# Performance work log

Measured on AMD Instinct MI355X. Metric: run time of the kernel, lower is better.

The kernel has to match this reference:

```python
import jax, jax.numpy as jnp
import numpy as np

B, N, D = 512, 22, 3
H, TD, AD, L = 128, 32, 32, 4
SIGMA_DATA = 0.168
NORM_CONST = 1.0
E_IN = 2 * H + 1 + 2  # [h_i, h_j, radial, dist_sq, bond_mask]
NUM_ATOM_TYPES = 4
BONDS = [(0, 1), (1, 2), (1, 3), (1, 4), (4, 5), (4, 6), (6, 7), (6, 8), (8, 9), (8, 10),
         (10, 11), (10, 12), (10, 13), (8, 14), (14, 15), (14, 16), (16, 17), (16, 18),
         (18, 19), (18, 20), (18, 21)]
ATOM_TYPES = [0, 1, 0, 0, 1, 2, 3, 0, 1, 0, 1, 0, 0, 0, 1, 2, 3, 0, 1, 0, 0, 0]


def setup_inputs() -> dict:
    key = jax.random.key(0)
    ks = jax.random.split(key, 16)
    xt = jax.random.normal(ks[0], (B, N, D), jnp.float32)
    xt = xt - xt.mean(axis=1, keepdims=True)  # zero center of mass, per assert_mean_zero
    # EDM-style noise levels, strictly positive (log-normal as in compute_loss)
    t = jnp.exp(jax.random.normal(ks[1], (B,), jnp.float32) * 1.2 - 1.2)
    # fully connected edges without self-loops, batched with node offset b*N
    ii, jj = np.meshgrid(np.arange(N), np.arange(N), indexing='ij')
    msk = ii != jj
    ri, ci = ii[msk], jj[msk]  # (N*(N-1),)
    off = (np.arange(B) * N)[:, None]
    row = jnp.asarray((ri[None] + off).reshape(-1), jnp.int32)
    col = jnp.asarray((ci[None] + off).reshape(-1), jnp.int32)
    adj = np.zeros((N, N), np.float32)
    for a, b in BONDS:
        adj[a, b] = 1.0
        adj[b, a] = 1.0
    bond_mask = jnp.asarray(np.tile(adj[ri, ci], B)[:, None], jnp.float32)  # (E,1)
    atom_types = jnp.asarray(ATOM_TYPES, jnp.int32)

    def lin(k, fi, fo):
        return jax.random.normal(k, (fi, fo), jnp.float32) / np.sqrt(fi)

    def per_layer(k, fi, fo):
        return jax.random.normal(k, (L, fi, fo), jnp.float32) / np.sqrt(fi)

    z = lambda *s: jnp.zeros(s, jnp.float32)
    return dict(
        xt=xt, t=t,
        atom_table=jax.random.normal(ks[2], (NUM_ATOM_TYPES, AD), jnp.float32),
        bond_mask=bond_mask,
        W_in=lin(ks[3], TD + AD, H), b_in=z(H),
        ew1=per_layer(ks[4], E_IN, H), eb1=z(L, H),
        ew2=per_layer(ks[5], H, H), eb2=z(L, H),
        aw=per_layer(ks[6], H, 1), ab=z(L, 1),
        cw1=per_layer(ks[7], H, H), cb1=z(L, H),
        cw2=per_layer(ks[8], H, 1) * 0.1,  # coord head, no bias (xavier-small init)
        nw1=per_layer(ks[9], 2 * H, H), nb1=z(L, H),
        nw2=per_layer(ks[10], H, H), nb2=z(L, H),
        row=row, col=col, atom_types=atom_types,
    )


def _sinusoidal(u, dim):
    half = dim // 2
    freqs = jnp.exp(-jnp.log(10000.0) * jnp.arange(half, dtype=jnp.float32) / half)
    a = u[:, None] * freqs
    return jnp.concatenate([jnp.sin(a), jnp.cos(a)], axis=-1)


def reference(xt, t, atom_table, bond_mask, W_in, b_in, ew1, eb1, ew2, eb2,
              aw, ab, cw1, cb1, cw2, nw1, nb1, nw2, nb2, row, col, atom_types):
    BN = B * N
    act = jax.nn.silu
    # EDM preconditioning
    c_in = 1.0 / jnp.sqrt(t ** 2 + SIGMA_DATA ** 2)
    x = (xt * c_in[:, None, None]).reshape(BN, D)
    # node features: time embedding (broadcast per node) + atom-type embedding
    time_emb = jnp.repeat(_sinusoidal(jnp.log(t) / 4.0, TD), N, axis=0)  # (BN,TD)
    atom_emb = jnp.tile(atom_table[atom_types], (B, 1))                  # (BN,AD)
    h = jnp.concatenate([time_emb, atom_emb], axis=1) @ W_in + b_in      # (BN,H)
    # fixed edge attributes: squared distance at input scale + bond mask
    dist_sq0 = jnp.sum((x[row] - x[col]) ** 2, axis=1, keepdims=True)
    edge_attr = jnp.concatenate([dist_sq0, bond_mask], axis=1)           # (E,2)
    for l in range(L):
        diff = x[row] - x[col]                                           # (E,D)
        radial = jnp.sum(diff ** 2, axis=1, keepdims=True)               # (E,1)
        coord_diff = diff / (jnp.sqrt(radial) + NORM_CONST)
        m = jnp.concatenate([h[row], h[col], radial, edge_attr], axis=1)
        m = act(act(m @ ew1[l] + eb1[l]) @ ew2[l] + eb2[l])              # edge MLP (E,H)
        m = m * jax.nn.sigmoid(m @ aw[l] + ab[l])                        # attention gate
        trans = coord_diff * (act(m @ cw1[l] + cb1[l]) @ cw2[l])         # (E,D)
        x = x + jax.ops.segment_sum(trans, row, num_segments=BN)         # agg='sum'
        agg = jax.ops.segment_sum(m, row, num_segments=BN)               # (BN,H)
        h = h + (act(jnp.concatenate([h, agg], axis=1) @ nw1[l] + nb1[l]) @ nw2[l] + nb2[l])
    x_pred = x.reshape(B, N, D)
    x_pred = x_pred - x_pred.mean(axis=1, keepdims=True)                 # remove_mean
    c_skip = SIGMA_DATA ** 2 / (t ** 2 + SIGMA_DATA ** 2)
    c_out = t * SIGMA_DATA / jnp.sqrt(SIGMA_DATA ** 2 + t ** 2)
    return xt * c_skip[:, None, None] + x_pred * c_out[:, None, None]
```

## Files before the change

### kernel.cpp

```cpp
#include <hip/hip_runtime.h>
#include <math.h>

#define NB 512
#define NNODE 22
#define HH 128
#define NEDGE 462
#define NLAYER 4
#define CHUNK2 128
#define NSUP 4
#define SIG 0.168f

#define ASTR 136
#define NSTR 264
#define BSTR 72
#define SLW (128*72)
#define LSLICES 14
#define STAGE_BYTES 36864

typedef __attribute__((ext_vector_type(8))) short short8;
typedef __attribute__((ext_vector_type(4))) short short4v;
typedef __attribute__((ext_vector_type(4))) float f32x4;

#define MFMA_BF16 __builtin_amdgcn_mfma_f32_16x16x32_bf16

__device__ __forceinline__ float siluf(float v) { return v / (1.0f + __expf(-v)); }

__device__ __forceinline__ unsigned short f2bf(float x) {
  union { float f; unsigned u; } v; v.f = x;
  unsigned r = v.u + 0x7FFFu + ((v.u >> 16) & 1u);
  return (unsigned short)(r >> 16);
}
__device__ __forceinline__ float bf2f(unsigned short h) {
  union { unsigned u; float f; } v; v.u = ((unsigned)h) << 16; return v.f;
}
__device__ __forceinline__ void splitbf(float x, unsigned short& hi, unsigned short& lo) {
  union { float f; unsigned u; } v; v.f = x;
  hi = (unsigned short)(v.u >> 16);
  union { unsigned u; float f; } hv; hv.u = ((unsigned)hi) << 16;
  union { float f; unsigned u; } w; w.f = x - hv.f;
  lo = (unsigned short)(w.u >> 16);
}

__global__ void prep_weights(const float* __restrict__ ew1, const float* __restrict__ ew2,
                             const float* __restrict__ cw1, const float* __restrict__ nw1,
                             const float* __restrict__ nw2, unsigned short* __restrict__ ws)
{
  int idx = blockIdx.x * 256 + threadIdx.x;
  if (idx >= 4 * LSLICES * 128 * 72) return;
  int kk = idx % 72; int rest = idx / 72;
  int n = rest % 128; rest /= 128;
  int sl = rest % LSLICES; int l = rest / LSLICES;
  float val = 0.f;
  if (kk < 64) {
    if (sl < 4)       val = ew1[((size_t)l * 259 + sl * 64 + kk) * HH + n];
    else if (sl < 6)  val = ew2[((size_t)l * 128 + (sl - 4) * 64 + kk) * HH + n];
    else if (sl < 8)  val = cw1[((size_t)l * 128 + (sl - 6) * 64 + kk) * HH + n];
    else if (sl < 12) val = nw1[((size_t)l * 256 + (sl - 8) * 64 + kk) * HH + n];
    else              val = nw2[((size_t)l * 128 + (sl - 12) * 64 + kk) * HH + n];
  }
  unsigned short hi, lo;
  { union { float f; unsigned u; } v; v.f = val;
    hi = (unsigned short)(v.u >> 16);
    union { unsigned u; float f; } hv; hv.u = ((unsigned)hi) << 16;
    lo = f2bf(val - hv.f); }
  size_t base = ((size_t)(l * LSLICES + sl) * 2) * SLW + n * BSTR + kk;
  ws[base]       = hi;
  ws[base + SLW] = lo;
}

__global__ __launch_bounds__(512, 1)
void scorenet_kernel(
    const float* __restrict__ xt, const float* __restrict__ tt,
    const float* __restrict__ atom_table, const float* __restrict__ bond_mask,
    const float* __restrict__ W_in, const float* __restrict__ b_in,
    const float* __restrict__ ew1, const float* __restrict__ eb1,
    const float* __restrict__ eb2,
    const float* __restrict__ aw,  const float* __restrict__ ab,
    const float* __restrict__ cb1, const float* __restrict__ cw2,
    const float* __restrict__ nb1, const float* __restrict__ nb2,
    const int* __restrict__ atom_types,
    const unsigned short* __restrict__ ws,
    float* __restrict__ out)
{
  const int g    = blockIdx.x;
  const int tid  = threadIdx.x;
  const int lane = tid & 63;
  const int wv   = tid >> 6;
  const int ml   = lane & 15;
  const int q    = lane >> 4;
  const int mp   = wv >> 1;
  const int nh2  = wv & 1;
  const int mtn  = wv & 1;
  const int nqn  = wv >> 1;

  __shared__ __align__(16) unsigned short sh_B[2 * SLW];
  __shared__ __align__(16) unsigned short sh_Ah[CHUNK2 * ASTR];
  __shared__ __align__(16) unsigned short sh_Al[CHUNK2 * ASTR];
  __shared__ float sh_Phi[2][NNODE * HH];
  __shared__ float sh_h[NNODE * HH];
  __shared__ float sh_agg[NNODE * HH];
  __shared__ float sh_tail[8 * HH];
  __shared__ float sh_awl[HH], sh_cw2l[HH];
  __shared__ float sh_x[NNODE][3], sh_xacc[NNODE][3];
  __shared__ float sh_d0[NEDGE];
  __shared__ unsigned char sh_ei[NEDGE];
  __shared__ unsigned char sh_ej[NEDGE];
  __shared__ float sh_cd[3][CHUNK2];
  __shared__ float sh_red[CHUNK2][2];
  __shared__ float sh_gate[CHUNK2];
  __shared__ float sh_tf[32], sh_scal[2], sh_mean[3];

  auto issueB = [&](const unsigned short* src) {
    const char* s8 = (const char*)src;
    char* dbase = (char*)&sh_B[0];
    for (int base = wv * 1024; base < STAGE_BYTES; base += 8192) {
      __builtin_amdgcn_global_load_lds(
          (const __attribute__((address_space(1))) unsigned int*)(s8 + base + lane * 16),
          (__attribute__((address_space(3))) unsigned int*)(dbase + base),
          16, 0, 0);
    }
  };

  auto gemmE = [&](f32x4 (&acc)[2][4], int koff) {
    int arow0 = (mp * 32 + ml) * ASTR + koff;
    int arow1 = arow0 + 16 * ASTR;
#pragma unroll
    for (int sb = 0; sb < 2; sb++) {
      int k8 = sb * 32 + q * 8;
      short8 ah0 = *(const short8*)&sh_Ah[arow0 + k8];
      short8 al0 = *(const short8*)&sh_Al[arow0 + k8];
      short8 ah1 = *(const short8*)&sh_Ah[arow1 + k8];
      short8 al1 = *(const short8*)&sh_Al[arow1 + k8];
#pragma unroll
      for (int t = 0; t < 4; t++) {
        int bi = ((nh2 * 4 + t) * 16 + ml) * BSTR + k8;
        short8 bh = *(const short8*)&sh_B[bi];
        short8 bl = *(const short8*)&sh_B[SLW + bi];
        acc[0][t] = MFMA_BF16(ah0, bh, acc[0][t], 0, 0, 0);
        acc[0][t] = MFMA_BF16(ah0, bl, acc[0][t], 0, 0, 0);
        acc[0][t] = MFMA_BF16(al0, bh, acc[0][t], 0, 0, 0);
        acc[1][t] = MFMA_BF16(ah1, bh, acc[1][t], 0, 0, 0);
        acc[1][t] = MFMA_BF16(ah1, bl, acc[1][t], 0, 0, 0);
        acc[1][t] = MFMA_BF16(al1, bh, acc[1][t], 0, 0, 0);
      }
    }
  };

  auto gemmN = [&](f32x4 (&acc)[2], int astr, int koff) {
#pragma unroll
    for (int sb = 0; sb < 2; sb++) {
      int ak = (mtn * 16 + ml) * astr + koff + sb * 32 + q * 8;
      short8 ah = *(const short8*)&sh_Ah[ak];
      short8 al = *(const short8*)&sh_Al[ak];
#pragma unroll
      for (int tt = 0; tt < 2; tt++) {
        int bi = ((nqn * 2 + tt) * 16 + ml) * BSTR + sb * 32 + q * 8;
        short8 bh = *(const short8*)&sh_B[bi];
        short8 bl = *(const short8*)&sh_B[SLW + bi];
        acc[tt] = MFMA_BF16(ah, bh, acc[tt], 0, 0, 0);
        acc[tt] = MFMA_BF16(ah, bl, acc[tt], 0, 0, 0);
        acc[tt] = MFMA_BF16(al, bh, acc[tt], 0, 0, 0);
      }
    }
  };

  if (tid == 0) {
    float tg = tt[g];
    sh_scal[0] = rsqrtf(tg * tg + SIG * SIG);
    sh_scal[1] = tg;
  }
  __syncthreads();
  const float c_in = sh_scal[0];
  for (int idx = tid; idx < NNODE * 3; idx += 512) {
    sh_x[idx / 3][idx % 3] = xt[(size_t)g * NNODE * 3 + idx] * c_in;
    sh_xacc[idx / 3][idx % 3] = 0.f;
  }
  if (tid < 32) {
    float u = __logf(sh_scal[1]) * 0.25f;
    int   qq = tid & 15;
    float f = __expf((float)qq * -0.5756462732485115f);
    float a = u * f;
    sh_tf[tid] = (tid < 16) ? __sinf(a) : __cosf(a);
  }
  for (int idx = tid; idx < CHUNK2 * ASTR / 2; idx += 512) {
    ((unsigned*)sh_Ah)[idx] = 0u; ((unsigned*)sh_Al)[idx] = 0u;
  }
  __syncthreads();
  for (int o = tid; o < HH; o += 512) {
    float s = b_in[o];
#pragma unroll 8
    for (int k = 0; k < 32; k++) s += sh_tf[k] * W_in[k * HH + o];
    sh_agg[o] = s;
  }
  for (int idx = tid; idx < 4 * HH; idx += 512) {
    int a = idx >> 7, o = idx & 127;
    float s = 0.f;
#pragma unroll 8
    for (int k = 0; k < 32; k++) s += atom_table[a * 32 + k] * W_in[(32 + k) * HH + o];
    sh_agg[(1 + a) * HH + o] = s;
  }
  for (int e = tid; e < NEDGE; e += 512) {
    int i = e / 21; int r = e - i * 21; int jn = r + (r >= i);
    float bm = bond_mask[(size_t)g * NEDGE + e];
    sh_ei[e] = (unsigned char)(i | ((bm != 0.f) ? 0x80 : 0));
    sh_ej[e] = (unsigned char)jn;
    float dx = sh_x[i][0] - sh_x[jn][0];
    float dy = sh_x[i][1] - sh_x[jn][1];
    float dz = sh_x[i][2] - sh_x[jn][2];
    sh_d0[e] = dx * dx + dy * dy + dz * dz;
  }
  __syncthreads();
  for (int idx = tid; idx < NNODE * HH; idx += 512) {
    int n = idx >> 7, o = idx & 127;
    int at = atom_types[n];
    sh_h[idx] = sh_agg[o] + sh_agg[(1 + at) * HH + o];
  }
  issueB(ws);
  __syncthreads();
  for (int idx = tid; idx < NNODE * HH; idx += 512) sh_agg[idx] = 0.f;

  const f32x4 zf = {0.f, 0.f, 0.f, 0.f};

  for (int l = 0; l < NLAYER; l++) {
    const unsigned short* wsL = ws + (size_t)l * LSLICES * 2 * SLW;
    const float abl = ab[l];

    for (int idx = tid; idx < 8 * HH; idx += 512) {
      int rsel = idx >> 7, n = idx & 127;
      float v;
      switch (rsel) {
        case 0: v = ew1[((size_t)l * 259 + 256) * HH + n]; break;
        case 1: v = ew1[((size_t)l * 259 + 257) * HH + n]; break;
        case 2: v = ew1[((size_t)l * 259 + 258) * HH + n]; break;
        case 3: v = eb1[l * HH + n]; break;
        case 4: v = eb2[l * HH + n]; break;
        case 5: v = cb1[l * HH + n]; break;
        case 6: v = nb1[l * HH + n]; break;
        default: v = nb2[l * HH + n]; break;
      }
      sh_tail[idx] = v;
    }
    if (tid < HH) sh_awl[tid] = aw[l * HH + tid];
    else if (tid < 2 * HH) sh_cw2l[tid - HH] = cw2[l * HH + (tid - HH)];
    for (int idx = tid; idx < NNODE * 16; idx += 512) {
      int nd = idx >> 4, nb = (idx & 15) * 8;
      const float* hp = &sh_h[nd * HH + nb];
      union { short8 v; unsigned short s[8]; } oh, ol;
#pragma unroll
      for (int jj = 0; jj < 8; jj++) { unsigned short hi, lo; splitbf(hp[jj], hi, lo); oh.s[jj] = hi; ol.s[jj] = lo; }
      *(short8*)&sh_Ah[nd * ASTR + nb] = oh.v;
      *(short8*)&sh_Al[nd * ASTR + nb] = ol.v;
    }
    __syncthreads();

    for (int side = 0; side < 2; side++) {
      f32x4 accP[2] = {zf, zf};
      for (int s2 = 0; s2 < 2; s2++) {
        gemmN(accP, ASTR, s2 * 64);
        __syncthreads();
        int st = side * 2 + s2;
        issueB(wsL + (st < 3 ? (st + 1) : 4) * 2 * SLW);
        if (s2 == 0) __syncthreads();
      }
#pragma unroll
      for (int tt = 0; tt < 2; tt++) {
        int col = (nqn * 2 + tt) * 16 + ml;
#pragma unroll
        for (int r = 0; r < 4; r++) {
          int row = mtn * 16 + q * 4 + r;
          if (row < NNODE) sh_Phi[side][row * HH + col] = accP[tt][r];
        }
      }
      __syncthreads();
    }

    for (int sc = 0; sc < NSUP; sc++) {
      const int e0 = sc * CHUNK2;
      {
        int nb = (tid & 15) * 8, eb_ = tid >> 4;
        for (int j4 = 0; j4 < 4; j4++) {
          int el = eb_ + 32 * j4; int e = e0 + el;
          union { short8 v; unsigned short s[8]; } oh, ol;
          if (e < NEDGE) {
            int c = sh_ei[e]; int i = c & 31; int jn = sh_ej[e];
            float bnd = (float)(c >> 7);
            float dx = sh_x[i][0] - sh_x[jn][0];
            float dy = sh_x[i][1] - sh_x[jn][1];
            float dz = sh_x[i][2] - sh_x[jn][2];
            float rad = dx * dx + dy * dy + dz * dz;
            float d0v = sh_d0[e];
            const float* pi = &sh_Phi[0][i * HH + nb];
            const float* pj = &sh_Phi[1][jn * HH + nb];
#pragma unroll
            for (int jj = 0; jj < 8; jj++) {
              float v = pi[jj] + pj[jj] +
                        rad * sh_tail[nb + jj] + d0v * sh_tail[128 + nb + jj] +
                        bnd * sh_tail[256 + nb + jj] + sh_tail[384 + nb + jj];
              unsigned short hi, lo; splitbf(siluf(v), hi, lo);
              oh.s[jj] = hi; ol.s[jj] = lo;
            }
          } else {
#pragma unroll
            for (int jj = 0; jj < 8; jj++) { oh.s[jj] = 0; ol.s[jj] = 0; }
          }
          *(short8*)&sh_Ah[el * ASTR + nb] = oh.v;
          *(short8*)&sh_Al[el * ASTR + nb] = ol.v;
        }
      }
      __syncthreads();
      f32x4 acc2[2][4];
#pragma unroll
      for (int m2i = 0; m2i < 2; m2i++)
#pragma unroll
        for (int t = 0; t < 4; t++) acc2[m2i][t] = zf;
      gemmE(acc2, 0);
      __syncthreads();
      issueB(wsL + 5 * 2 * SLW);
      if (tid < CHUNK2) {
        int e = e0 + tid;
        if (e < NEDGE) {
          int i = sh_ei[e] & 31, jn = sh_ej[e];
          float dx = sh_x[i][0] - sh_x[jn][0];
          float dy = sh_x[i][1] - sh_x[jn][1];
          float dz = sh_x[i][2] - sh_x[jn][2];
          float inv = 1.0f / (sqrtf(dx * dx + dy * dy + dz * dz) + 1.0f);
          sh_cd[0][tid] = dx * inv; sh_cd[1][tid] = dy * inv; sh_cd[2][tid] = dz * inv;
        } else {
          sh_cd[0][tid] = 0.f; sh_cd[1][tid] = 0.f; sh_cd[2][tid] = 0.f;
        }
      }
      __syncthreads();
      gemmE(acc2, 64);
      __syncthreads();
      issueB(wsL + 6 * 2 * SLW);
      {
        float gpr[2][4];
#pragma unroll
        for (int m2i = 0; m2i < 2; m2i++)
#pragma unroll
          for (int r = 0; r < 4; r++) gpr[m2i][r] = 0.f;
#pragma unroll
        for (int m2i = 0; m2i < 2; m2i++) {
#pragma unroll
          for (int t = 0; t < 4; t++) {
            int col = nh2 * 64 + t * 16 + ml;
            float eb2c = sh_tail[512 + col], awc = sh_awl[col];
#pragma unroll
            for (int r = 0; r < 4; r++) {
              float v = siluf(acc2[m2i][t][r] + eb2c);
              gpr[m2i][r] += v * awc;
              unsigned short hi, lo; splitbf(v, hi, lo);
              int ai = (mp * 32 + m2i * 16 + q * 4 + r) * ASTR + col;
              sh_Ah[ai] = hi; sh_Al[ai] = lo;
            }
          }
        }
#pragma unroll
        for (int m = 1; m < 16; m <<= 1)
#pragma unroll
          for (int m2i = 0; m2i < 2; m2i++)
#pragma unroll
            for (int r = 0; r < 4; r++) gpr[m2i][r] += __shfl_xor(gpr[m2i][r], m, 64);
        if (ml == 0) {
#pragma unroll
          for (int m2i = 0; m2i < 2; m2i++)
#pragma unroll
            for (int r = 0; r < 4; r++)
              sh_red[mp * 32 + m2i * 16 + q * 4 + r][nh2] = gpr[m2i][r];
        }
      }
      __syncthreads();
      if (tid < CHUNK2)
        sh_gate[tid] = 1.0f / (1.0f + __expf(-(sh_red[tid][0] + sh_red[tid][1] + abl)));
      f32x4 acc3[2][4];
#pragma unroll
      for (int m2i = 0; m2i < 2; m2i++)
#pragma unroll
        for (int t = 0; t < 4; t++) acc3[m2i][t] = zf;
      gemmE(acc3, 0);
      __syncthreads();
      issueB(wsL + 7 * 2 * SLW);
      int elast = ((e0 + CHUNK2 < NEDGE) ? e0 + CHUNK2 : NEDGE) - 1;
      int i_lo = e0 / 21, i_hi = elast / 21;
      int nrows = i_hi - i_lo + 1;
      for (int idx = tid; idx < nrows * 32; idx += 512) {
        int i = i_lo + (idx >> 5), fb = (idx & 31) * 4;
        int es = i * 21; if (es < e0) es = e0;
        int ee = i * 21 + 21;
        if (ee > e0 + CHUNK2) ee = e0 + CHUNK2;
        if (ee > NEDGE) ee = NEDGE;
        float* ap = &sh_agg[i * HH + fb];
        float a4[4];
#pragma unroll
        for (int c = 0; c < 4; c++) a4[c] = ap[c];
        for (int e = es; e < ee; e++) {
          float gg = sh_gate[e - e0];
          union { short4v v; unsigned short s[4]; } uh, ul;
          uh.v = *(const short4v*)&sh_Ah[(e - e0) * ASTR + fb];
          ul.v = *(const short4v*)&sh_Al[(e - e0) * ASTR + fb];
#pragma unroll
          for (int c = 0; c < 4; c++) a4[c] += gg * (bf2f(uh.s[c]) + bf2f(ul.s[c]));
        }
#pragma unroll
        for (int c = 0; c < 4; c++) ap[c] = a4[c];
      }
      __syncthreads();
      gemmE(acc3, 64);
      __syncthreads();
      issueB(sc < 3 ? wsL + 4 * 2 * SLW : wsL + 8 * 2 * SLW);
      {
        float cs[2][4];
#pragma unroll
        for (int m2i = 0; m2i < 2; m2i++) {
          float g4[4];
#pragma unroll
          for (int r = 0; r < 4; r++) {
            g4[r] = sh_gate[mp * 32 + m2i * 16 + q * 4 + r];
            cs[m2i][r] = 0.f;
          }
#pragma unroll
          for (int t = 0; t < 4; t++) {
            int col = nh2 * 64 + t * 16 + ml;
            float cb1c = sh_tail[640 + col], cwc = sh_cw2l[col];
#pragma unroll
            for (int r = 0; r < 4; r++)
              cs[m2i][r] += siluf(g4[r] * acc3[m2i][t][r] + cb1c) * cwc;
          }
        }
#pragma unroll
        for (int m = 1; m < 16; m <<= 1)
#pragma unroll
          for (int m2i = 0; m2i < 2; m2i++)
#pragma unroll
            for (int r = 0; r < 4; r++) cs[m2i][r] += __shfl_xor(cs[m2i][r], m, 64);
        if (ml == 0) {
#pragma unroll
          for (int m2i = 0; m2i < 2; m2i++)
#pragma unroll
            for (int r = 0; r < 4; r++)
              sh_red[mp * 32 + m2i * 16 + q * 4 + r][nh2] = cs[m2i][r];
        }
      }
      __syncthreads();
      for (int idx = tid; idx < nrows * 3; idx += 512) {
        int i = i_lo + idx / 3, d = idx % 3;
        int es = i * 21; if (es < e0) es = e0;
        int ee = i * 21 + 21;
        if (ee > e0 + CHUNK2) ee = e0 + CHUNK2;
        if (ee > NEDGE) ee = NEDGE;
        float s = 0.f;
        for (int e = es; e < ee; e++)
          s += sh_cd[d][e - e0] * (sh_red[e - e0][0] + sh_red[e - e0][1]);
        sh_xacc[i][d] += s;
      }
    }

    for (int idx = tid; idx < NNODE * 32; idx += 512) {
      int nd = idx >> 5, kb = (idx & 31) * 8;
      const float* src = (kb < 128) ? &sh_h[nd * HH + kb] : &sh_agg[nd * HH + (kb - 128)];
      union { short8 v; unsigned short s[8]; } oh, ol;
#pragma unroll
      for (int jj = 0; jj < 8; jj++) { unsigned short hi, lo; splitbf(src[jj], hi, lo); oh.s[jj] = hi; ol.s[jj] = lo; }
      *(short8*)&sh_Ah[nd * NSTR + kb] = oh.v;
      *(short8*)&sh_Al[nd * NSTR + kb] = ol.v;
    }
    __syncthreads();
    {
      f32x4 n1a[2] = {zf, zf};
      for (int s = 0; s < 4; s++) {
        gemmN(n1a, NSTR, s * 64);
        __syncthreads();
        issueB(wsL + (s < 3 ? (9 + s) : 12) * 2 * SLW);
        if (s < 3) __syncthreads();
      }
#pragma unroll
      for (int tt = 0; tt < 2; tt++) {
        int col = (nqn * 2 + tt) * 16 + ml;
        float nb1c = sh_tail[768 + col];
#pragma unroll
        for (int r = 0; r < 4; r++) {
          int row = mtn * 16 + q * 4 + r;
          if (row < NNODE) {
            unsigned short hi, lo; splitbf(siluf(n1a[tt][r] + nb1c), hi, lo);
            sh_Ah[row * ASTR + col] = hi; sh_Al[row * ASTR + col] = lo;
          }
        }
      }
      __syncthreads();
      f32x4 n2a[2] = {zf, zf};
      gemmN(n2a, ASTR, 0);
      __syncthreads();
      issueB(wsL + 13 * 2 * SLW);
      for (int idx = tid; idx < NNODE * 3; idx += 512) {
        int n = idx / 3, d = idx % 3;
        sh_x[n][d] += sh_xacc[n][d];
        sh_xacc[n][d] = 0.f;
      }
      for (int idx = tid; idx < NNODE * HH; idx += 512) sh_agg[idx] = 0.f;
      __syncthreads();
      gemmN(n2a, ASTR, 64);
      __syncthreads();
      if (l < 3) issueB(ws + (size_t)(l + 1) * LSLICES * 2 * SLW);
#pragma unroll
      for (int tt = 0; tt < 2; tt++) {
        int col = (nqn * 2 + tt) * 16 + ml;
        float nb2c = sh_tail[896 + col];
#pragma unroll
        for (int r = 0; r < 4; r++) {
          int row = mtn * 16 + q * 4 + r;
          if (row < NNODE) sh_h[row * HH + col] += n2a[tt][r] + nb2c;
        }
      }
    }
    __syncthreads();
  }

  if (tid < 3) {
    float s = 0.f;
    for (int n = 0; n < NNODE; n++) s += sh_x[n][tid];
    sh_mean[tid] = s * (1.0f / NNODE);
  }
  __syncthreads();
  {
    float tg = sh_scal[1];
    float den = tg * tg + SIG * SIG;
    float c_skip = (SIG * SIG) / den;
    float c_out  = tg * SIG * rsqrtf(den);
    for (int idx = tid; idx < NNODE * 3; idx += 512) {
      int n = idx / 3, d = idx % 3;
      out[(size_t)g * NNODE * 3 + idx] =
          xt[(size_t)g * NNODE * 3 + idx] * c_skip + (sh_x[n][d] - sh_mean[d]) * c_out;
    }
  }
}

extern "C" void kernel_launch(void* const* d_in, const int* in_sizes, int n_in,
                              void* d_out, int out_size, void* d_ws, size_t ws_size,
                              hipStream_t stream) {
  const float* xt         = (const float*)d_in[0];
  const float* t          = (const float*)d_in[1];
  const float* atom_table = (const float*)d_in[2];
  const float* bond_mask  = (const float*)d_in[3];
  const float* W_in       = (const float*)d_in[4];
  const float* b_in       = (const float*)d_in[5];
  const float* ew1        = (const float*)d_in[6];
  const float* eb1        = (const float*)d_in[7];
  const float* ew2        = (const float*)d_in[8];
  const float* eb2        = (const float*)d_in[9];
  const float* aw         = (const float*)d_in[10];
  const float* ab         = (const float*)d_in[11];
  const float* cw1        = (const float*)d_in[12];
  const float* cb1        = (const float*)d_in[13];
  const float* cw2        = (const float*)d_in[14];
  const float* nw1        = (const float*)d_in[15];
  const float* nb1        = (const float*)d_in[16];
  const float* nw2        = (const float*)d_in[17];
  const float* nb2        = (const float*)d_in[18];
  const int* atom_types   = (const int*)d_in[21];

  unsigned short* ws = (unsigned short*)d_ws;

  prep_weights<<<2016, 256, 0, stream>>>(ew1, ew2, cw1, nw1, nw2, ws);

  scorenet_kernel<<<NB, 512, 0, stream>>>(
      xt, t, atom_table, bond_mask, W_in, b_in,
      ew1, eb1, eb2, aw, ab, cb1, cw2, nb1, nb2,
      atom_types, ws, (float*)d_out);
}
```

Measured before the change: 703.0 us.

## Double block size to 1024 threads and re-split MFMA tiles across 16 waves

Raises the block from 8 to 16 waves and remaps the edge and node GEMM tiles so each wave owns half as many output columns, with the gate and coordinate reductions widened to four partial sums. It also drops the precomputed initial-distance array and instead recomputes the initial squared distance per edge from a saved copy of the initial coordinates. The aim is more latency hiding and MFMA parallelism per CU for the single resident block. In exchange, the register budget per thread is tighter, barrier cost rises with more waves, and each wave now loads the A fragments for only half the MFMAs.

```diff
diff --git a/kernel.cpp b/kernel.cpp
--- a/kernel.cpp
+++ b/kernel.cpp
@@ -16,6 +16,7 @@
 #define SLW (128*72)
 #define LSLICES 14
 #define STAGE_BYTES 36864
+#define NT 1024
 
 typedef __attribute__((ext_vector_type(8))) short short8;
 typedef __attribute__((ext_vector_type(4))) short short4v;
@@ -68,7 +69,7 @@
   ws[base + SLW] = lo;
 }
 
-__global__ __launch_bounds__(512, 1)
+__global__ __launch_bounds__(NT, 1)
 void scorenet_kernel(
     const float* __restrict__ xt, const float* __restrict__ tt,
     const float* __restrict__ atom_table, const float* __restrict__ bond_mask,
@@ -88,10 +89,10 @@
   const int wv   = tid >> 6;
   const int ml   = lane & 15;
   const int q    = lane >> 4;
-  const int mp   = wv >> 1;
-  const int nh2  = wv & 1;
+  const int mp   = wv >> 2;
+  const int nq   = wv & 3;
   const int mtn  = wv & 1;
-  const int nqn  = wv >> 1;
+  const int nt8  = wv >> 1;
 
   __shared__ __align__(16) unsigned short sh_B[2 * SLW];
   __shared__ __align__(16) unsigned short sh_Ah[CHUNK2 * ASTR];
@@ -101,19 +102,18 @@
   __shared__ float sh_agg[NNODE * HH];
   __shared__ float sh_tail[8 * HH];
   __shared__ float sh_awl[HH], sh_cw2l[HH];
-  __shared__ float sh_x[NNODE][3], sh_xacc[NNODE][3];
-  __shared__ float sh_d0[NEDGE];
+  __shared__ float sh_x[NNODE][3], sh_xacc[NNODE][3], sh_x0[NNODE][3];
   __shared__ unsigned char sh_ei[NEDGE];
   __shared__ unsigned char sh_ej[NEDGE];
   __shared__ float sh_cd[3][CHUNK2];
-  __shared__ float sh_red[CHUNK2][2];
+  __shared__ float sh_red[CHUNK2][4];
   __shared__ float sh_gate[CHUNK2];
   __shared__ float sh_tf[32], sh_scal[2], sh_mean[3];
 
   auto issueB = [&](const unsigned short* src) {
     const char* s8 = (const char*)src;
     char* dbase = (char*)&sh_B[0];
-    for (int base = wv * 1024; base < STAGE_BYTES; base += 8192) {
+    for (int base = wv * 1024; base < STAGE_BYTES; base += 16384) {
       __builtin_amdgcn_global_load_lds(
           (const __attribute__((address_space(1))) unsigned int*)(s8 + base + lane * 16),
           (__attribute__((address_space(3))) unsigned int*)(dbase + base),
@@ -121,7 +121,7 @@
     }
   };
 
-  auto gemmE = [&](f32x4 (&acc)[2][4], int koff) {
+  auto gemmE = [&](f32x4 (&acc)[2][2], int koff) {
     int arow0 = (mp * 32 + ml) * ASTR + koff;
     int arow1 = arow0 + 16 * ASTR;
 #pragma unroll
@@ -132,8 +132,8 @@
       short8 ah1 = *(const short8*)&sh_Ah[arow1 + k8];
       short8 al1 = *(const short8*)&sh_Al[arow1 + k8];
 #pragma unroll
-      for (int t = 0; t < 4; t++) {
-        int bi = ((nh2 * 4 + t) * 16 + ml) * BSTR + k8;
+      for (int t = 0; t < 2; t++) {
+        int bi = ((nq * 2 + t) * 16 + ml) * BSTR + k8;
         short8 bh = *(const short8*)&sh_B[bi];
         short8 bl = *(const short8*)&sh_B[SLW + bi];
         acc[0][t] = MFMA_BF16(ah0, bh, acc[0][t], 0, 0, 0);
@@ -146,21 +146,18 @@
     }
   };
 
-  auto gemmN = [&](f32x4 (&acc)[2], int astr, int koff) {
+  auto gemmN = [&](f32x4& acc, int astr, int koff) {
 #pragma unroll
     for (int sb = 0; sb < 2; sb++) {
       int ak = (mtn * 16 + ml) * astr + koff + sb * 32 + q * 8;
       short8 ah = *(const short8*)&sh_Ah[ak];
       short8 al = *(const short8*)&sh_Al[ak];
-#pragma unroll
-      for (int tt = 0; tt < 2; tt++) {
-        int bi = ((nqn * 2 + tt) * 16 + ml) * BSTR + sb * 32 + q * 8;
-        short8 bh = *(const short8*)&sh_B[bi];
-        short8 bl = *(const short8*)&sh_B[SLW + bi];
-        acc[tt] = MFMA_BF16(ah, bh, acc[tt], 0, 0, 0);
-        acc[tt] = MFMA_BF16(ah, bl, acc[tt], 0, 0, 0);
-        acc[tt] = MFMA_BF16(al, bh, acc[tt], 0, 0, 0);
-      }
+      int bi = (nt8 * 16 + ml) * BSTR + sb * 32 + q * 8;
+      short8 bh = *(const short8*)&sh_B[bi];
+      short8 bl = *(const short8*)&sh_B[SLW + bi];
+      acc = MFMA_BF16(ah, bh, acc, 0, 0, 0);
+      acc = MFMA_BF16(ah, bl, acc, 0, 0, 0);
+      acc = MFMA_BF16(al, bh, acc, 0, 0, 0);
     }
   };
 
@@ -171,8 +168,10 @@
   }
   __syncthreads();
   const float c_in = sh_scal[0];
-  for (int idx = tid; idx < NNODE * 3; idx += 512) {
-    sh_x[idx / 3][idx % 3] = xt[(size_t)g * NNODE * 3 + idx] * c_in;
+  for (int idx = tid; idx < NNODE * 3; idx += NT) {
+    float xv = xt[(size_t)g * NNODE * 3 + idx] * c_in;
+    sh_x[idx / 3][idx % 3] = xv;
+    sh_x0[idx / 3][idx % 3] = xv;
     sh_xacc[idx / 3][idx % 3] = 0.f;
   }
   if (tid < 32) {
@@ -182,42 +181,38 @@
     float a = u * f;
     sh_tf[tid] = (tid < 16) ? __sinf(a) : __cosf(a);
   }
-  for (int idx = tid; idx < CHUNK2 * ASTR / 2; idx += 512) {
+  for (int idx = tid; idx < CHUNK2 * ASTR / 2; idx += NT) {
     ((unsigned*)sh_Ah)[idx] = 0u; ((unsigned*)sh_Al)[idx] = 0u;
   }
+  for (int e = tid; e < NEDGE; e += NT) {
+    int i = e / 21; int r = e - i * 21; int jn = r + (r >= i);
+    float bm = bond_mask[(size_t)g * NEDGE + e];
+    sh_ei[e] = (unsigned char)(i | ((bm != 0.f) ? 0x80 : 0));
+    sh_ej[e] = (unsigned char)jn;
+  }
   __syncthreads();
-  for (int o = tid; o < HH; o += 512) {
+  for (int o = tid; o < HH; o += NT) {
     float s = b_in[o];
 #pragma unroll 8
     for (int k = 0; k < 32; k++) s += sh_tf[k] * W_in[k * HH + o];
     sh_agg[o] = s;
   }
-  for (int idx = tid; idx < 4 * HH; idx += 512) {
+  for (int idx = tid; idx < 4 * HH; idx += NT) {
     int a = idx >> 7, o = idx & 127;
     float s = 0.f;
 #pragma unroll 8
     for (int k = 0; k < 32; k++) s += atom_table[a * 32 + k] * W_in[(32 + k) * HH + o];
     sh_agg[(1 + a) * HH + o] = s;
   }
-  for (int e = tid; e < NEDGE; e += 512) {
-    int i = e / 21; int r = e - i * 21; int jn = r + (r >= i);
-    float bm = bond_mask[(size_t)g * NEDGE + e];
-    sh_ei[e] = (unsigned char)(i | ((bm != 0.f) ? 0x80 : 0));
-    sh_ej[e] = (unsigned char)jn;
-    float dx = sh_x[i][0] - sh_x[jn][0];
-    float dy = sh_x[i][1] - sh_x[jn][1];
-    float dz = sh_x[i][2] - sh_x[jn][2];
-    sh_d0[e] = dx * dx + dy * dy + dz * dz;
-  }
   __syncthreads();
-  for (int idx = tid; idx < NNODE * HH; idx += 512) {
+  for (int idx = tid; idx < NNODE * HH; idx += NT) {
     int n = idx >> 7, o = idx & 127;
     int at = atom_types[n];
     sh_h[idx] = sh_agg[o] + sh_agg[(1 + at) * HH + o];
   }
   issueB(ws);
   __syncthreads();
-  for (int idx = tid; idx < NNODE * HH; idx += 512) sh_agg[idx] = 0.f;
+  for (int idx = tid; idx < NNODE * HH; idx += NT) sh_agg[idx] = 0.f;
 
   const f32x4 zf = {0.f, 0.f, 0.f, 0.f};
 
@@ -225,7 +220,7 @@
     const unsigned short* wsL = ws + (size_t)l * LSLICES * 2 * SLW;
     const float abl = ab[l];
 
-    for (int idx = tid; idx < 8 * HH; idx += 512) {
+    for (int idx = tid; idx < 8 * HH; idx += NT) {
       int rsel = idx >> 7, n = idx & 127;
       float v;
       switch (rsel) {
@@ -242,7 +237,7 @@
     }
     if (tid < HH) sh_awl[tid] = aw[l * HH + tid];
     else if (tid < 2 * HH) sh_cw2l[tid - HH] = cw2[l * HH + (tid - HH)];
-    for (int idx = tid; idx < NNODE * 16; idx += 512) {
+    for (int idx = tid; idx < NNODE * 16; idx += NT) {
       int nd = idx >> 4, nb = (idx & 15) * 8;
       const float* hp = &sh_h[nd * HH + nb];
       union { short8 v; unsigned short s[8]; } oh, ol;
@@ -254,7 +249,7 @@
     __syncthreads();
 
     for (int side = 0; side < 2; side++) {
-      f32x4 accP[2] = {zf, zf};
+      f32x4 accP = zf;
       for (int s2 = 0; s2 < 2; s2++) {
         gemmN(accP, ASTR, s2 * 64);
         __syncthreads();
@@ -262,13 +257,12 @@
         issueB(wsL + (st < 3 ? (st + 1) : 4) * 2 * SLW);
         if (s2 == 0) __syncthreads();
       }
-#pragma unroll
-      for (int tt = 0; tt < 2; tt++) {
-        int col = (nqn * 2 + tt) * 16 + ml;
+      {
+        int col = nt8 * 16 + ml;
 #pragma unroll
         for (int r = 0; r < 4; r++) {
           int row = mtn * 16 + q * 4 + r;
-          if (row < NNODE) sh_Phi[side][row * HH + col] = accP[tt][r];
+          if (row < NNODE) sh_Phi[side][row * HH + col] = accP[r];
         }
       }
       __syncthreads();
@@ -278,8 +272,8 @@
       const int e0 = sc * CHUNK2;
       {
         int nb = (tid & 15) * 8, eb_ = tid >> 4;
-        for (int j4 = 0; j4 < 4; j4++) {
-          int el = eb_ + 32 * j4; int e = e0 + el;
+        for (int j4 = 0; j4 < 2; j4++) {
+          int el = eb_ + 64 * j4; int e = e0 + el;
           union { short8 v; unsigned short s[8]; } oh, ol;
           if (e < NEDGE) {
             int c = sh_ei[e]; int i = c & 31; int jn = sh_ej[e];
@@ -288,7 +282,10 @@
             float dy = sh_x[i][1] - sh_x[jn][1];
             float dz = sh_x[i][2] - sh_x[jn][2];
             float rad = dx * dx + dy * dy + dz * dz;
-            float d0v = sh_d0[e];
+            float ex = sh_x0[i][0] - sh_x0[jn][0];
+            float ey = sh_x0[i][1] - sh_x0[jn][1];
+            float ez = sh_x0[i][2] - sh_x0[jn][2];
+            float d0v = ex * ex + ey * ey + ez * ez;
             const float* pi = &sh_Phi[0][i * HH + nb];
             const float* pj = &sh_Phi[1][jn * HH + nb];
 #pragma unroll
@@ -308,11 +305,11 @@
         }
       }
       __syncthreads();
-      f32x4 acc2[2][4];
+      f32x4 acc2[2][2];
 #pragma unroll
       for (int m2i = 0; m2i < 2; m2i++)
 #pragma unroll
-        for (int t = 0; t < 4; t++) acc2[m2i][t] = zf;
+        for (int t = 0; t < 2; t++) acc2[m2i][t] = zf;
       gemmE(acc2, 0);
       __syncthreads();
       issueB(wsL + 5 * 2 * SLW);
@@ -342,8 +339,8 @@
 #pragma unroll
         for (int m2i = 0; m2i < 2; m2i++) {
 #pragma unroll
-          for (int t = 0; t < 4; t++) {
-            int col = nh2 * 64 + t * 16 + ml;
+          for (int t = 0; t < 2; t++) {
+            int col = nq * 32 + t * 16 + ml;
             float eb2c = sh_tail[512 + col], awc = sh_awl[col];
 #pragma unroll
             for (int r = 0; r < 4; r++) {
@@ -366,24 +363,25 @@
           for (int m2i = 0; m2i < 2; m2i++)
 #pragma unroll
             for (int r = 0; r < 4; r++)
-              sh_red[mp * 32 + m2i * 16 + q * 4 + r][nh2] = gpr[m2i][r];
+              sh_red[mp * 32 + m2i * 16 + q * 4 + r][nq] = gpr[m2i][r];
         }
       }
       __syncthreads();
       if (tid < CHUNK2)
-        sh_gate[tid] = 1.0f / (1.0f + __expf(-(sh_red[tid][0] + sh_red[tid][1] + abl)));
-      f32x4 acc3[2][4];
+        sh_gate[tid] = 1.0f / (1.0f + __expf(-(sh_red[tid][0] + sh_red[tid][1] +
+                                               sh_red[tid][2] + sh_red[tid][3] + abl)));
+      f32x4 acc3[2][2];
 #pragma unroll
       for (int m2i = 0; m2i < 2; m2i++)
 #pragma unroll
-        for (int t = 0; t < 4; t++) acc3[m2i][t] = zf;
+        for (int t = 0; t < 2; t++) acc3[m2i][t] = zf;
       gemmE(acc3, 0);
       __syncthreads();
       issueB(wsL + 7 * 2 * SLW);
       int elast = ((e0 + CHUNK2 < NEDGE) ? e0 + CHUNK2 : NEDGE) - 1;
       int i_lo = e0 / 21, i_hi = elast / 21;
       int nrows = i_hi - i_lo + 1;
-      for (int idx = tid; idx < nrows * 32; idx += 512) {
+      for (int idx = tid; idx < nrows * 32; idx += NT) {
         int i = i_lo + (idx >> 5), fb = (idx & 31) * 4;
         int es = i * 21; if (es < e0) es = e0;
         int ee = i * 21 + 21;
@@ -419,8 +417,8 @@
             cs[m2i][r] = 0.f;
           }
 #pragma unroll
-          for (int t = 0; t < 4; t++) {
-            int col = nh2 * 64 + t * 16 + ml;
+          for (int t = 0; t < 2; t++) {
+            int col = nq * 32 + t * 16 + ml;
             float cb1c = sh_tail[640 + col], cwc = sh_cw2l[col];
 #pragma unroll
             for (int r = 0; r < 4; r++)
@@ -438,24 +436,26 @@
           for (int m2i = 0; m2i < 2; m2i++)
 #pragma unroll
             for (int r = 0; r < 4; r++)
-              sh_red[mp * 32 + m2i * 16 + q * 4 + r][nh2] = cs[m2i][r];
-        }
-      }
-      __syncthreads();
-      for (int idx = tid; idx < nrows * 3; idx += 512) {
+              sh_red[mp * 32 + m2i * 16 + q * 4 + r][nq] = cs[m2i][r];
+        }
+      }
+      __syncthreads();
+      for (int idx = tid; idx < nrows * 3; idx += NT) {
         int i = i_lo + idx / 3, d = idx % 3;
         int es = i * 21; if (es < e0) es = e0;
         int ee = i * 21 + 21;
         if (ee > e0 + CHUNK2) ee = e0 + CHUNK2;
         if (ee > NEDGE) ee = NEDGE;
         float s = 0.f;
-        for (int e = es; e < ee; e++)
-          s += sh_cd[d][e - e0] * (sh_red[e - e0][0] + sh_red[e - e0][1]);
+        for (int e = es; e < ee; e++) {
+          const float* rd = sh_red[e - e0];
+          s += sh_cd[d][e - e0] * (rd[0] + rd[1] + rd[2] + rd[3]);
+        }
         sh_xacc[i][d] += s;
       }
     }
 
-    for (int idx = tid; idx < NNODE * 32; idx += 512) {
+    for (int idx = tid; idx < NNODE * 32; idx += NT) {
       int nd = idx >> 5, kb = (idx & 31) * 8;
       const float* src = (kb < 128) ? &sh_h[nd * HH + kb] : &sh_agg[nd * HH + (kb - 128)];
       union { short8 v; unsigned short s[8]; } oh, ol;
@@ -466,49 +466,47 @@
     }
     __syncthreads();
     {
-      f32x4 n1a[2] = {zf, zf};
+      f32x4 n1a = zf;
       for (int s = 0; s < 4; s++) {
         gemmN(n1a, NSTR, s * 64);
         __syncthreads();
         issueB(wsL + (s < 3 ? (9 + s) : 12) * 2 * SLW);
         if (s < 3) __syncthreads();
       }
-#pragma unroll
-      for (int tt = 0; tt < 2; tt++) {
-        int col = (nqn * 2 + tt) * 16 + ml;
+      {
+        int col = nt8 * 16 + ml;
         float nb1c = sh_tail[768 + col];
 #pragma unroll
         for (int r = 0; r < 4; r++) {
           int row = mtn * 16 + q * 4 + r;
           if (row < NNODE) {
-            unsigned short hi, lo; splitbf(siluf(n1a[tt][r] + nb1c), hi, lo);
+            unsigned short hi, lo; splitbf(siluf(n1a[r] + nb1c), hi, lo);
             sh_Ah[row * ASTR + col] = hi; sh_Al[row * ASTR + col] = lo;
           }
         }
       }
       __syncthreads();
-      f32x4 n2a[2] = {zf, zf};
+      f32x4 n2a = zf;
       gemmN(n2a, ASTR, 0);
       __syncthreads();
       issueB(wsL + 13 * 2 * SLW);
-      for (int idx = tid; idx < NNODE * 3; idx += 512) {
+      for (int idx = tid; idx < NNODE * 3; idx += NT) {
         int n = idx / 3, d = idx % 3;
         sh_x[n][d] += sh_xacc[n][d];
         sh_xacc[n][d] = 0.f;
       }
-      for (int idx = tid; idx < NNODE * HH; idx += 512) sh_agg[idx] = 0.f;
+      for (int idx = tid; idx < NNODE * HH; idx += NT) sh_agg[idx] = 0.f;
       __syncthreads();
       gemmN(n2a, ASTR, 64);
       __syncthreads();
       if (l < 3) issueB(ws + (size_t)(l + 1) * LSLICES * 2 * SLW);
-#pragma unroll
-      for (int tt = 0; tt < 2; tt++) {
-        int col = (nqn * 2 + tt) * 16 + ml;
+      {
+        int col = nt8 * 16 + ml;
         float nb2c = sh_tail[896 + col];
 #pragma unroll
         for (int r = 0; r < 4; r++) {
           int row = mtn * 16 + q * 4 + r;
-          if (row < NNODE) sh_h[row * HH + col] += n2a[tt][r] + nb2c;
+          if (row < NNODE) sh_h[row * HH + col] += n2a[r] + nb2c;
         }
       }
     }
@@ -526,7 +524,7 @@
     float den = tg * tg + SIG * SIG;
     float c_skip = (SIG * SIG) / den;
     float c_out  = tg * SIG * rsqrtf(den);
-    for (int idx = tid; idx < NNODE * 3; idx += 512) {
+    for (int idx = tid; idx < NNODE * 3; idx += NT) {
       int n = idx / 3, d = idx % 3;
       out[(size_t)g * NNODE * 3 + idx] =
           xt[(size_t)g * NNODE * 3 + idx] * c_skip + (sh_x[n][d] - sh_mean[d]) * c_out;
@@ -562,7 +560,7 @@
 
   prep_weights<<<2016, 256, 0, stream>>>(ew1, ew2, cw1, nw1, nw2, ws);
 
-  scorenet_kernel<<<NB, 512, 0, stream>>>(
+  scorenet_kernel<<<NB, NT, 0, stream>>>(
       xt, t, atom_table, bond_mask, W_in, b_in,
       ew1, eb1, eb2, aw, ab, cb1, cw2, nb1, nb2,
       atom_types, ws, (float*)d_out);
```

Result: slower. 751.7 us (+6.9%).
